# Kernel tuning notes

Measured on AMD Instinct MI355X. Metric: run time of the kernel, lower is better.

## Reference

```python
import jax, jax.numpy as jnp
import numpy as np

B, S, D = 2, 2048, 1024
H, DK = 16, 64  # n_heads, d_k == d_v


def setup_inputs() -> dict:
    key = jax.random.key(0)
    ks = jax.random.split(key, 12)
    sd = 1.0 / np.sqrt(D)
    inp = {
        "Q": jax.random.normal(ks[0], (B, S, D), jnp.float32),
        "K": jax.random.normal(ks[1], (B, S, D), jnp.float32),
        "V": jax.random.normal(ks[2], (B, S, D), jnp.float32),
        "attn_mask": jax.random.randint(ks[3], (B, S, S), 0, 2).astype(bool),
        "Wq": jax.random.normal(ks[4], (D, H * DK), jnp.float32) * sd,
        "bq": jnp.zeros((H * DK,), jnp.float32),
        "Wk": jax.random.normal(ks[5], (D, H * DK), jnp.float32) * sd,
        "bk": jnp.zeros((H * DK,), jnp.float32),
        "Wv": jax.random.normal(ks[6], (D, H * DK), jnp.float32) * sd,
        "bv": jnp.zeros((H * DK,), jnp.float32),
        "Wo": jax.random.normal(ks[7], (H * DK, D), jnp.float32) * sd,
        "bo": jnp.zeros((D,), jnp.float32),
        "ln_g": jnp.ones((D,), jnp.float32),
        "ln_b": jnp.zeros((D,), jnp.float32),
    }
    return inp


def _layer_norm(x, g, b, eps=1e-5):
    mu = jnp.mean(x, axis=-1, keepdims=True)
    var = jnp.var(x, axis=-1, keepdims=True)
    return (x - mu) * jax.lax.rsqrt(var + eps) * g + b


def reference(Q, K, V, attn_mask, Wq, bq, Wk, bk, Wv, bv, Wo, bo, ln_g, ln_b):
    # NOTE: faithful to the source — K and V projections are computed from Q.
    residual = Q
    q = (Q @ Wq + bq).reshape(B, S, H, DK).transpose(0, 2, 1, 3)  # [B,H,S,DK]
    k = (Q @ Wk + bk).reshape(B, S, H, DK).transpose(0, 2, 1, 3)
    v = (Q @ Wv + bv).reshape(B, S, H, DK).transpose(0, 2, 1, 3)
    scale = 1.0 / np.sqrt(DK)
    scores = jnp.einsum("bhqd,bhkd->bhqk", q, k) * scale  # [B,H,S,S]
    scores = jnp.where(attn_mask[:, None, :, :], jnp.float32(-1e9), scores)
    attn = jax.nn.softmax(scores, axis=-1)
    context = jnp.einsum("bhqk,bhkd->bhqd", attn, v)
    context = context.transpose(0, 2, 1, 3).reshape(B, S, H * DK)
    output = context @ Wo + bo
    return _layer_norm(output + residual, ln_g, ln_b), attn
```

## Files before the change

### kernel.cpp

```cpp
#include <hip/hip_runtime.h>
#include <stdint.h>

typedef unsigned short u16;
typedef short bf16x8 __attribute__((ext_vector_type(8)));
typedef float f32x4 __attribute__((ext_vector_type(4)));

static __device__ __forceinline__ u16 f2b(float f) {
    uint32_t u = __float_as_uint(f);
    uint32_t r = (u + 0x7fffu + ((u >> 16) & 1u)) >> 16;
    return (u16)r;
}
static __device__ __forceinline__ float b2f(u16 u) {
    union { float f; uint32_t i; } x; x.i = ((uint32_t)u) << 16; return x.f;
}

__global__ __launch_bounds__(256) void pack_mask_k(const int* __restrict__ mask,
                                                   unsigned long long* __restrict__ bits) {
    const int row = blockIdx.x;
    const int wave = threadIdx.x >> 6, lane = threadIdx.x & 63;
    const int* mrow = mask + (size_t)row * 2048;
#pragma unroll
    for (int it = 0; it < 8; ++it) {
        int col = it * 256 + threadIdx.x;
        unsigned long long b = __ballot(mrow[col] != 0);
        if (lane == 0) bits[(size_t)row * 32 + it * 4 + wave] = b;
    }
}

__global__ __launch_bounds__(256) void transpose_w_k(const float* __restrict__ Wq, const float* __restrict__ Wk,
                                                     const float* __restrict__ Wv, const float* __restrict__ Wo,
                                                     u16* __restrict__ WtAll) {
    __shared__ u16 t[32][36];
    const float* W = blockIdx.z == 0 ? Wq : blockIdx.z == 1 ? Wk : blockIdx.z == 2 ? Wv : Wo;
    u16* out = WtAll + (size_t)blockIdx.z * (1024u * 1024u);
    const int r = threadIdx.x >> 3, c4 = (threadIdx.x & 7) * 4;
    float4 v = *(const float4*)(W + (size_t)(blockIdx.y * 32 + r) * 1024 + blockIdx.x * 32 + c4);
    t[r][c4 + 0] = f2b(v.x); t[r][c4 + 1] = f2b(v.y); t[r][c4 + 2] = f2b(v.z); t[r][c4 + 3] = f2b(v.w);
    __syncthreads();
    ushort4 o;
    o.x = t[c4 + 0][r]; o.y = t[c4 + 1][r]; o.z = t[c4 + 2][r]; o.w = t[c4 + 3][r];
    *(ushort4*)(out + (size_t)(blockIdx.x * 32 + r) * 1024 + blockIdx.y * 32 + c4) = o;
}

__global__ __launch_bounds__(256) void proj_qkv_k(const float* __restrict__ Q, const u16* __restrict__ WtAll,
                                                  const float* __restrict__ bq, const float* __restrict__ bk,
                                                  const float* __restrict__ bv,
                                                  u16* __restrict__ q_ws, u16* __restrict__ k_ws,
                                                  u16* __restrict__ v_ws) {
    const int z = blockIdx.z;
    const u16* Bt = WtAll + (size_t)z * (1024u * 1024u);
    const float* bias = z == 0 ? bq : z == 1 ? bk : bv;
    u16* out = z == 0 ? q_ws : z == 1 ? k_ws : v_ws;
    const float oscale = (z == 0) ? 0.18033688011112042f : 1.0f;

    __shared__ u16 Asm[64][40];
    __shared__ u16 Bsm[64][40];

    const int tid = threadIdx.x;
    const int wave = tid >> 6, lane = tid & 63, quad = lane >> 4, l16 = lane & 15;
    const int m0 = blockIdx.y * 64, n0 = blockIdx.x * 64;
    const int srow = tid >> 2, scol = (tid & 3) * 8;

    const float* Ag = Q + (size_t)(m0 + srow) * 1024 + scol;
    const u16* Bg = Bt + (size_t)(n0 + srow) * 1024 + scol;

    const f32x4 zero = {0.f, 0.f, 0.f, 0.f};
    f32x4 acc[4];
#pragma unroll
    for (int i = 0; i < 4; ++i) acc[i] = zero;

    for (int k0 = 0; k0 < 1024; k0 += 32) {
        float4 a0 = *(const float4*)(Ag + k0);
        float4 a1 = *(const float4*)(Ag + k0 + 4);
        u16* asl = &Asm[srow][scol];
        asl[0] = f2b(a0.x); asl[1] = f2b(a0.y); asl[2] = f2b(a0.z); asl[3] = f2b(a0.w);
        asl[4] = f2b(a1.x); asl[5] = f2b(a1.y); asl[6] = f2b(a1.z); asl[7] = f2b(a1.w);
        *(bf16x8*)&Bsm[srow][scol] = *(const bf16x8*)(Bg + k0);
        __syncthreads();
        bf16x8 a = *(const bf16x8*)&Asm[wave * 16 + l16][quad * 8];
#pragma unroll
        for (int nt = 0; nt < 4; ++nt) {
            bf16x8 bb = *(const bf16x8*)&Bsm[nt * 16 + l16][quad * 8];
            acc[nt] = __builtin_amdgcn_mfma_f32_16x16x32_bf16(a, bb, acc[nt], 0, 0, 0);
        }
        __syncthreads();
    }

    const int h = blockIdx.x;
#pragma unroll
    for (int nt = 0; nt < 4; ++nt) {
        const int d = nt * 16 + l16;
        const float bsf = bias[h * 64 + d];
#pragma unroll
        for (int r = 0; r < 4; ++r) {
            const int m = m0 + wave * 16 + quad * 4 + r;
            const int bb = m >> 11, s = m & 2047;
            out[((size_t)(bb * 16 + h) * 2048 + s) * 64 + d] = f2b((acc[nt][r] + bsf) * oscale);
        }
    }
}

__global__ __launch_bounds__(256) void attn_k(const u16* __restrict__ q_ws, const u16* __restrict__ k_ws,
                                              const u16* __restrict__ v_ws,
                                              const unsigned long long* __restrict__ mbits,
                                              float* __restrict__ attn_out, u16* __restrict__ ctx_ws) {
    const int bh = blockIdx.y, b = bh >> 4, h = bh & 15;
    const int q0 = blockIdx.x * 64;
    const int tid = threadIdx.x;
    const int wave = tid >> 6, lane = tid & 63, quad = lane >> 4, l16 = lane & 15;

    __shared__ u16 Ksm[64][72];
    __shared__ u16 Vsm[64][72];
    __shared__ u16 Psm[4][16][72];

    const u16* qp = q_ws + ((size_t)bh * 2048 + q0 + wave * 16 + l16) * 64;
    const bf16x8 aq0 = *(const bf16x8*)(qp + quad * 8);
    const bf16x8 aq1 = *(const bf16x8*)(qp + 32 + quad * 8);

    const size_t mbase = ((size_t)b * 2048 + q0 + wave * 16 + quad * 4) * 32;

    const int r0 = tid >> 3, c0 = (tid & 7) * 8;
    const u16* kgb = k_ws + (size_t)bh * 2048 * 64;
    const u16* vgb = v_ws + (size_t)bh * 2048 * 64;

    const f32x4 zero = {0.f, 0.f, 0.f, 0.f};
    float lsum[4] = {0.f, 0.f, 0.f, 0.f};

    for (int kt = 0; kt < 32; ++kt) {
        const int s0 = kt * 64;
        *(bf16x8*)&Ksm[r0][c0] = *(const bf16x8*)(kgb + (size_t)(s0 + r0) * 64 + c0);
        *(bf16x8*)&Ksm[r0 + 32][c0] = *(const bf16x8*)(kgb + (size_t)(s0 + r0 + 32) * 64 + c0);
        __syncthreads();
        f32x4 sc[4];
#pragma unroll
        for (int nt = 0; nt < 4; ++nt) {
            sc[nt] = zero;
            bf16x8 bk0 = *(const bf16x8*)&Ksm[nt * 16 + l16][quad * 8];
            bf16x8 bk1 = *(const bf16x8*)&Ksm[nt * 16 + l16][32 + quad * 8];
            sc[nt] = __builtin_amdgcn_mfma_f32_16x16x32_bf16(aq0, bk0, sc[nt], 0, 0, 0);
            sc[nt] = __builtin_amdgcn_mfma_f32_16x16x32_bf16(aq1, bk1, sc[nt], 0, 0, 0);
        }
        unsigned long long mw[4];
#pragma unroll
        for (int r = 0; r < 4; ++r) mw[r] = mbits[mbase + (size_t)r * 32 + kt];
#pragma unroll
        for (int nt = 0; nt < 4; ++nt)
#pragma unroll
            for (int r = 0; r < 4; ++r) {
                const int bit = (int)((mw[r] >> (nt * 16 + l16)) & 1ull);
                lsum[r] += bit ? 0.f : exp2f(sc[nt][r]);
            }
        __syncthreads();
    }
#pragma unroll
    for (int r = 0; r < 4; ++r) {
#pragma unroll
        for (int off = 1; off < 16; off <<= 1) lsum[r] += __shfl_xor(lsum[r], off, 64);
    }
    float rl[4];
#pragma unroll
    for (int r = 0; r < 4; ++r) rl[r] = 1.0f / lsum[r];

    f32x4 cacc[4];
#pragma unroll
    for (int i = 0; i < 4; ++i) cacc[i] = zero;

    for (int kt = 0; kt < 32; ++kt) {
        const int s0 = kt * 64;
        *(bf16x8*)&Ksm[r0][c0] = *(const bf16x8*)(kgb + (size_t)(s0 + r0) * 64 + c0);
        *(bf16x8*)&Ksm[r0 + 32][c0] = *(const bf16x8*)(kgb + (size_t)(s0 + r0 + 32) * 64 + c0);
        bf16x8 v0 = *(const bf16x8*)(vgb + (size_t)(s0 + r0) * 64 + c0);
        bf16x8 v1 = *(const bf16x8*)(vgb + (size_t)(s0 + r0 + 32) * 64 + c0);
#pragma unroll
        for (int j = 0; j < 8; ++j) {
            Vsm[c0 + j][r0] = (u16)v0[j];
            Vsm[c0 + j][r0 + 32] = (u16)v1[j];
        }
        __syncthreads();

        f32x4 sc[4];
#pragma unroll
        for (int nt = 0; nt < 4; ++nt) {
            sc[nt] = zero;
            bf16x8 bk0 = *(const bf16x8*)&Ksm[nt * 16 + l16][quad * 8];
            bf16x8 bk1 = *(const bf16x8*)&Ksm[nt * 16 + l16][32 + quad * 8];
            sc[nt] = __builtin_amdgcn_mfma_f32_16x16x32_bf16(aq0, bk0, sc[nt], 0, 0, 0);
            sc[nt] = __builtin_amdgcn_mfma_f32_16x16x32_bf16(aq1, bk1, sc[nt], 0, 0, 0);
        }
        unsigned long long mw[4];
#pragma unroll
        for (int r = 0; r < 4; ++r) mw[r] = mbits[mbase + (size_t)r * 32 + kt];
#pragma unroll
        for (int nt = 0; nt < 4; ++nt)
#pragma unroll
            for (int r = 0; r < 4; ++r) {
                const int bit = (int)((mw[r] >> (nt * 16 + l16)) & 1ull);
                const float p = bit ? 0.f : exp2f(sc[nt][r]) * rl[r];
                Psm[wave][quad * 4 + r][nt * 16 + l16] = f2b(p);
            }
#pragma unroll
        for (int j = 0; j < 4; ++j) {
            const int pr = j * 4 + (lane >> 4), pc = (lane & 15) * 4;
            ushort4 pv = *(const ushort4*)&Psm[wave][pr][pc];
            float4 pf;
            pf.x = b2f(pv.x); pf.y = b2f(pv.y); pf.z = b2f(pv.z); pf.w = b2f(pv.w);
            float* ap = attn_out + ((size_t)bh * 2048 + q0 + wave * 16 + pr) * 2048 + s0 + pc;
            *(float4*)ap = pf;
        }
        bf16x8 pa0 = *(const bf16x8*)&Psm[wave][l16][quad * 8];
        bf16x8 pa1 = *(const bf16x8*)&Psm[wave][l16][32 + quad * 8];
#pragma unroll
        for (int dt = 0; dt < 4; ++dt) {
            bf16x8 bv0 = *(const bf16x8*)&Vsm[dt * 16 + l16][quad * 8];
            bf16x8 bv1 = *(const bf16x8*)&Vsm[dt * 16 + l16][32 + quad * 8];
            cacc[dt] = __builtin_amdgcn_mfma_f32_16x16x32_bf16(pa0, bv0, cacc[dt], 0, 0, 0);
            cacc[dt] = __builtin_amdgcn_mfma_f32_16x16x32_bf16(pa1, bv1, cacc[dt], 0, 0, 0);
        }
        __syncthreads();
    }

#pragma unroll
    for (int dt = 0; dt < 4; ++dt) {
        const int d = dt * 16 + l16;
#pragma unroll
        for (int r = 0; r < 4; ++r) {
            const int s = q0 + wave * 16 + quad * 4 + r;
            ctx_ws[((size_t)b * 2048 + s) * 1024 + h * 64 + d] = f2b(cacc[dt][r]);
        }
    }
}

__global__ __launch_bounds__(256) void out_proj_k(const u16* __restrict__ Ctx, const u16* __restrict__ WtO,
                                                  const float* __restrict__ bo, const float* __restrict__ Qin,
                                                  float* __restrict__ ln_in) {
    __shared__ u16 Asm[64][40];
    __shared__ u16 Bsm[64][40];
    const int tid = threadIdx.x;
    const int wave = tid >> 6, lane = tid & 63, quad = lane >> 4, l16 = lane & 15;
    const int m0 = blockIdx.y * 64, n0 = blockIdx.x * 64;
    const int srow = tid >> 2, scol = (tid & 3) * 8;
    const u16* Ag = Ctx + (size_t)(m0 + srow) * 1024 + scol;
    const u16* Bg = WtO + (size_t)(n0 + srow) * 1024 + scol;

    const f32x4 zero = {0.f, 0.f, 0.f, 0.f};
    f32x4 acc[4];
#pragma unroll
    for (int i = 0; i < 4; ++i) acc[i] = zero;

    for (int k0 = 0; k0 < 1024; k0 += 32) {
        *(bf16x8*)&Asm[srow][scol] = *(const bf16x8*)(Ag + k0);
        *(bf16x8*)&Bsm[srow][scol] = *(const bf16x8*)(Bg + k0);
        __syncthreads();
        bf16x8 a = *(const bf16x8*)&Asm[wave * 16 + l16][quad * 8];
#pragma unroll
        for (int nt = 0; nt < 4; ++nt) {
            bf16x8 bb = *(const bf16x8*)&Bsm[nt * 16 + l16][quad * 8];
            acc[nt] = __builtin_amdgcn_mfma_f32_16x16x32_bf16(a, bb, acc[nt], 0, 0, 0);
        }
        __syncthreads();
    }
#pragma unroll
    for (int nt = 0; nt < 4; ++nt) {
        const int n = n0 + nt * 16 + l16;
        const float bsf = bo[n];
#pragma unroll
        for (int r = 0; r < 4; ++r) {
            const int m = m0 + wave * 16 + quad * 4 + r;
            ln_in[(size_t)m * 1024 + n] = acc[nt][r] + bsf + Qin[(size_t)m * 1024 + n];
        }
    }
}

__global__ __launch_bounds__(256) void layernorm_k(const float* __restrict__ x, const float* __restrict__ g,
                                                   const float* __restrict__ bta, float* __restrict__ out) {
    const int row = blockIdx.x, tid = threadIdx.x;
    const float4 v = *(const float4*)(x + (size_t)row * 1024 + tid * 4);
    float s = v.x + v.y + v.z + v.w;
    float sq = v.x * v.x + v.y * v.y + v.z * v.z + v.w * v.w;
#pragma unroll
    for (int off = 32; off; off >>= 1) {
        s += __shfl_xor(s, off, 64);
        sq += __shfl_xor(sq, off, 64);
    }
    __shared__ float ss[4], ssq[4];
    const int wave = tid >> 6, lane = tid & 63;
    if (lane == 0) { ss[wave] = s; ssq[wave] = sq; }
    __syncthreads();
    const float S = ss[0] + ss[1] + ss[2] + ss[3];
    const float SQ = ssq[0] + ssq[1] + ssq[2] + ssq[3];
    const float mu = S * (1.f / 1024.f);
    const float rs = rsqrtf(SQ * (1.f / 1024.f) - mu * mu + 1e-5f);
    const float* vf = (const float*)&v;
    float4 o;
    float tmp[4];
#pragma unroll
    for (int j = 0; j < 4; ++j) {
        const int c = tid * 4 + j;
        tmp[j] = (vf[j] - mu) * rs * g[c] + bta[c];
    }
    o.x = tmp[0]; o.y = tmp[1]; o.z = tmp[2]; o.w = tmp[3];
    *(float4*)(out + (size_t)row * 1024 + tid * 4) = o;
}

extern "C" void kernel_launch(void* const* d_in, const int* in_sizes, int n_in,
                              void* d_out, int out_size, void* d_ws, size_t ws_size,
                              hipStream_t stream) {
    const float* Q  = (const float*)d_in[0];
    const int* mask = (const int*)d_in[3];
    const float* Wq = (const float*)d_in[4];
    const float* bq = (const float*)d_in[5];
    const float* Wk = (const float*)d_in[6];
    const float* bk = (const float*)d_in[7];
    const float* Wv = (const float*)d_in[8];
    const float* bv = (const float*)d_in[9];
    const float* Wo = (const float*)d_in[10];
    const float* bo = (const float*)d_in[11];
    const float* g  = (const float*)d_in[12];
    const float* be = (const float*)d_in[13];

    char* ws = (char*)d_ws;
    u16* WtAll = (u16*)(ws);
    u16* q_ws  = (u16*)(ws + ((size_t)8  << 20));
    u16* k_ws  = (u16*)(ws + ((size_t)16 << 20));
    u16* v_ws  = (u16*)(ws + ((size_t)24 << 20));
    u16* c_ws  = (u16*)(ws + ((size_t)32 << 20));
    float* ln_in = (float*)(ws + ((size_t)40 << 20));
    unsigned long long* mbits = (unsigned long long*)(ws + ((size_t)56 << 20));

    float* out_ln = (float*)d_out;
    float* out_at = (float*)d_out + (size_t)2 * 2048 * 1024;

    transpose_w_k<<<dim3(32, 32, 4), dim3(256), 0, stream>>>(Wq, Wk, Wv, Wo, WtAll);
    pack_mask_k<<<dim3(4096), dim3(256), 0, stream>>>(mask, mbits);
    proj_qkv_k<<<dim3(16, 64, 3), dim3(256), 0, stream>>>(Q, WtAll, bq, bk, bv, q_ws, k_ws, v_ws);
    attn_k<<<dim3(32, 32), dim3(256), 0, stream>>>(q_ws, k_ws, v_ws, mbits, out_at, c_ws);
    out_proj_k<<<dim3(16, 64), dim3(256), 0, stream>>>(c_ws, WtAll + (size_t)3 * 1024 * 1024, bo, Q, ln_in);
    layernorm_k<<<dim3(4096), dim3(256), 0, stream>>>(ln_in, g, be, out_ln);
    (void)in_sizes; (void)n_in; (void)out_size; (void)ws_size;
}
```

Measured before the change: 911.1 us.

## Use 128x128 GEMM tiles with direct global-to-LDS loads and pre-transposed V

Q is converted to bf16 once in a separate kernel. The QKV projection becomes one fused GEMM over the concatenated weights with 128x128 tiles, and both GEMMs load operands straight into LDS with global_load_lds. V is transposed in a dedicated kernel so the attention kernel can copy V tiles into LDS with vector stores instead of scattered per-element writes. This cuts global traffic and the fp32 conversion work inside the GEMM loops, at the cost of extra kernel launches and the workspace traffic for the intermediate buffers.

```diff
diff --git a/kernel.cpp b/kernel.cpp
--- a/kernel.cpp
+++ b/kernel.cpp
@@ -13,6 +13,11 @@
 static __device__ __forceinline__ float b2f(u16 u) {
     union { float f; uint32_t i; } x; x.i = ((uint32_t)u) << 16; return x.f;
 }
+
+#define GLOAD16(g, l)                                                        \
+    __builtin_amdgcn_global_load_lds(                                        \
+        (const __attribute__((address_space(1))) uint32_t*)(g),              \
+        (__attribute__((address_space(3))) uint32_t*)(l), 16, 0, 0)
 
 __global__ __launch_bounds__(256) void pack_mask_k(const int* __restrict__ mask,
                                                    unsigned long long* __restrict__ bits) {
@@ -42,66 +47,92 @@
     *(ushort4*)(out + (size_t)(blockIdx.x * 32 + r) * 1024 + blockIdx.y * 32 + c4) = o;
 }
 
-__global__ __launch_bounds__(256) void proj_qkv_k(const float* __restrict__ Q, const u16* __restrict__ WtAll,
+__global__ __launch_bounds__(256) void qcvt_k(const float* __restrict__ Q, u16* __restrict__ qbf) {
+    const size_t i = ((size_t)blockIdx.x * 256 + threadIdx.x) * 8;
+    float4 a = *(const float4*)(Q + i);
+    float4 b = *(const float4*)(Q + i + 4);
+    bf16x8 o;
+    o[0] = (short)f2b(a.x); o[1] = (short)f2b(a.y); o[2] = (short)f2b(a.z); o[3] = (short)f2b(a.w);
+    o[4] = (short)f2b(b.x); o[5] = (short)f2b(b.y); o[6] = (short)f2b(b.z); o[7] = (short)f2b(b.w);
+    *(bf16x8*)(qbf + i) = o;
+}
+
+__global__ __launch_bounds__(256) void gemm_qkv_k(const u16* __restrict__ Abf, const u16* __restrict__ WtAll,
                                                   const float* __restrict__ bq, const float* __restrict__ bk,
                                                   const float* __restrict__ bv,
                                                   u16* __restrict__ q_ws, u16* __restrict__ k_ws,
                                                   u16* __restrict__ v_ws) {
-    const int z = blockIdx.z;
-    const u16* Bt = WtAll + (size_t)z * (1024u * 1024u);
+    __shared__ u16 Asm[128 * 32];
+    __shared__ u16 Bsm[128 * 32];
+    const int tid = threadIdx.x;
+    const int wave = tid >> 6, lane = tid & 63, quad = lane >> 4, l16 = lane & 15;
+    const int wr = wave >> 1, wc = wave & 1;
+    const int m0 = blockIdx.y * 128, n0 = blockIdx.x * 128;
+
+    const u16* Ag = Abf + (size_t)(m0 + (tid >> 2)) * 1024 + (tid & 3) * 8;
+    const u16* Bg = WtAll + (size_t)(n0 + (tid >> 2)) * 1024 + (tid & 3) * 8;
+
+    const f32x4 zero = {0.f, 0.f, 0.f, 0.f};
+    f32x4 acc[4][4];
+#pragma unroll
+    for (int i = 0; i < 4; ++i)
+#pragma unroll
+        for (int j = 0; j < 4; ++j) acc[i][j] = zero;
+
+    for (int k0 = 0; k0 < 1024; k0 += 32) {
+        GLOAD16(Ag + k0, &Asm[tid * 8]);
+        GLOAD16(Ag + k0 + (size_t)64 * 1024, &Asm[2048 + tid * 8]);
+        GLOAD16(Bg + k0, &Bsm[tid * 8]);
+        GLOAD16(Bg + k0 + (size_t)64 * 1024, &Bsm[2048 + tid * 8]);
+        __syncthreads();
+        bf16x8 a[4], b[4];
+#pragma unroll
+        for (int i = 0; i < 4; ++i) {
+            a[i] = *(const bf16x8*)&Asm[(wr * 64 + i * 16 + l16) * 32 + quad * 8];
+            b[i] = *(const bf16x8*)&Bsm[(wc * 64 + i * 16 + l16) * 32 + quad * 8];
+        }
+#pragma unroll
+        for (int mi = 0; mi < 4; ++mi)
+#pragma unroll
+            for (int ni = 0; ni < 4; ++ni)
+                acc[mi][ni] = __builtin_amdgcn_mfma_f32_16x16x32_bf16(a[mi], b[ni], acc[mi][ni], 0, 0, 0);
+        __syncthreads();
+    }
+
+    const int z = n0 >> 10;
     const float* bias = z == 0 ? bq : z == 1 ? bk : bv;
     u16* out = z == 0 ? q_ws : z == 1 ? k_ws : v_ws;
     const float oscale = (z == 0) ? 0.18033688011112042f : 1.0f;
-
-    __shared__ u16 Asm[64][40];
-    __shared__ u16 Bsm[64][40];
-
-    const int tid = threadIdx.x;
-    const int wave = tid >> 6, lane = tid & 63, quad = lane >> 4, l16 = lane & 15;
-    const int m0 = blockIdx.y * 64, n0 = blockIdx.x * 64;
-    const int srow = tid >> 2, scol = (tid & 3) * 8;
-
-    const float* Ag = Q + (size_t)(m0 + srow) * 1024 + scol;
-    const u16* Bg = Bt + (size_t)(n0 + srow) * 1024 + scol;
-
-    const f32x4 zero = {0.f, 0.f, 0.f, 0.f};
-    f32x4 acc[4];
-#pragma unroll
-    for (int i = 0; i < 4; ++i) acc[i] = zero;
-
-    for (int k0 = 0; k0 < 1024; k0 += 32) {
-        float4 a0 = *(const float4*)(Ag + k0);
-        float4 a1 = *(const float4*)(Ag + k0 + 4);
-        u16* asl = &Asm[srow][scol];
-        asl[0] = f2b(a0.x); asl[1] = f2b(a0.y); asl[2] = f2b(a0.z); asl[3] = f2b(a0.w);
-        asl[4] = f2b(a1.x); asl[5] = f2b(a1.y); asl[6] = f2b(a1.z); asl[7] = f2b(a1.w);
-        *(bf16x8*)&Bsm[srow][scol] = *(const bf16x8*)(Bg + k0);
-        __syncthreads();
-        bf16x8 a = *(const bf16x8*)&Asm[wave * 16 + l16][quad * 8];
-#pragma unroll
-        for (int nt = 0; nt < 4; ++nt) {
-            bf16x8 bb = *(const bf16x8*)&Bsm[nt * 16 + l16][quad * 8];
-            acc[nt] = __builtin_amdgcn_mfma_f32_16x16x32_bf16(a, bb, acc[nt], 0, 0, 0);
-        }
-        __syncthreads();
-    }
-
-    const int h = blockIdx.x;
-#pragma unroll
-    for (int nt = 0; nt < 4; ++nt) {
-        const int d = nt * 16 + l16;
-        const float bsf = bias[h * 64 + d];
-#pragma unroll
-        for (int r = 0; r < 4; ++r) {
-            const int m = m0 + wave * 16 + quad * 4 + r;
-            const int bb = m >> 11, s = m & 2047;
-            out[((size_t)(bb * 16 + h) * 2048 + s) * 64 + d] = f2b((acc[nt][r] + bsf) * oscale);
-        }
-    }
+#pragma unroll
+    for (int ni = 0; ni < 4; ++ni) {
+        const int n = n0 + wc * 64 + ni * 16 + l16;
+        const int nn = n & 1023, h = nn >> 6, d = nn & 63;
+        const float bsf = bias[nn];
+#pragma unroll
+        for (int mi = 0; mi < 4; ++mi)
+#pragma unroll
+            for (int r = 0; r < 4; ++r) {
+                const int m = m0 + wr * 64 + mi * 16 + quad * 4 + r;
+                const int bb = m >> 11, s = m & 2047;
+                out[((size_t)(bb * 16 + h) * 2048 + s) * 64 + d] = f2b((acc[mi][ni][r] + bsf) * oscale);
+            }
+    }
+}
+
+__global__ __launch_bounds__(256) void vtr_k(const u16* __restrict__ v_ws, u16* __restrict__ vT) {
+    __shared__ u16 t[32][36];
+    const int bh = blockIdx.z, s0 = blockIdx.x * 32, d0 = blockIdx.y * 32;
+    const int r = threadIdx.x >> 3, c4 = (threadIdx.x & 7) * 4;
+    ushort4 v = *(const ushort4*)(v_ws + ((size_t)bh * 2048 + s0 + r) * 64 + d0 + c4);
+    t[r][c4 + 0] = v.x; t[r][c4 + 1] = v.y; t[r][c4 + 2] = v.z; t[r][c4 + 3] = v.w;
+    __syncthreads();
+    ushort4 o;
+    o.x = t[c4 + 0][r]; o.y = t[c4 + 1][r]; o.z = t[c4 + 2][r]; o.w = t[c4 + 3][r];
+    *(ushort4*)(vT + ((size_t)bh * 64 + d0 + r) * 2048 + s0 + c4) = o;
 }
 
 __global__ __launch_bounds__(256) void attn_k(const u16* __restrict__ q_ws, const u16* __restrict__ k_ws,
-                                              const u16* __restrict__ v_ws,
+                                              const u16* __restrict__ vT,
                                               const unsigned long long* __restrict__ mbits,
                                               float* __restrict__ attn_out, u16* __restrict__ ctx_ws) {
     const int bh = blockIdx.y, b = bh >> 4, h = bh & 15;
@@ -121,7 +152,7 @@
 
     const int r0 = tid >> 3, c0 = (tid & 7) * 8;
     const u16* kgb = k_ws + (size_t)bh * 2048 * 64;
-    const u16* vgb = v_ws + (size_t)bh * 2048 * 64;
+    const u16* vtg = vT + (size_t)bh * 64 * 2048;
 
     const f32x4 zero = {0.f, 0.f, 0.f, 0.f};
     float lsum[4] = {0.f, 0.f, 0.f, 0.f};
@@ -169,13 +200,8 @@
         const int s0 = kt * 64;
         *(bf16x8*)&Ksm[r0][c0] = *(const bf16x8*)(kgb + (size_t)(s0 + r0) * 64 + c0);
         *(bf16x8*)&Ksm[r0 + 32][c0] = *(const bf16x8*)(kgb + (size_t)(s0 + r0 + 32) * 64 + c0);
-        bf16x8 v0 = *(const bf16x8*)(vgb + (size_t)(s0 + r0) * 64 + c0);
-        bf16x8 v1 = *(const bf16x8*)(vgb + (size_t)(s0 + r0 + 32) * 64 + c0);
-#pragma unroll
-        for (int j = 0; j < 8; ++j) {
-            Vsm[c0 + j][r0] = (u16)v0[j];
-            Vsm[c0 + j][r0 + 32] = (u16)v1[j];
-        }
+        *(bf16x8*)&Vsm[r0][c0] = *(const bf16x8*)(vtg + (size_t)r0 * 2048 + s0 + c0);
+        *(bf16x8*)&Vsm[r0 + 32][c0] = *(const bf16x8*)(vtg + (size_t)(r0 + 32) * 2048 + s0 + c0);
         __syncthreads();
 
         f32x4 sc[4];
@@ -233,41 +259,53 @@
 __global__ __launch_bounds__(256) void out_proj_k(const u16* __restrict__ Ctx, const u16* __restrict__ WtO,
                                                   const float* __restrict__ bo, const float* __restrict__ Qin,
                                                   float* __restrict__ ln_in) {
-    __shared__ u16 Asm[64][40];
-    __shared__ u16 Bsm[64][40];
+    __shared__ u16 Asm[128 * 32];
+    __shared__ u16 Bsm[128 * 32];
     const int tid = threadIdx.x;
     const int wave = tid >> 6, lane = tid & 63, quad = lane >> 4, l16 = lane & 15;
-    const int m0 = blockIdx.y * 64, n0 = blockIdx.x * 64;
-    const int srow = tid >> 2, scol = (tid & 3) * 8;
-    const u16* Ag = Ctx + (size_t)(m0 + srow) * 1024 + scol;
-    const u16* Bg = WtO + (size_t)(n0 + srow) * 1024 + scol;
+    const int wr = wave >> 1, wc = wave & 1;
+    const int m0 = blockIdx.y * 128, n0 = blockIdx.x * 128;
+
+    const u16* Ag = Ctx + (size_t)(m0 + (tid >> 2)) * 1024 + (tid & 3) * 8;
+    const u16* Bg = WtO + (size_t)(n0 + (tid >> 2)) * 1024 + (tid & 3) * 8;
 
     const f32x4 zero = {0.f, 0.f, 0.f, 0.f};
-    f32x4 acc[4];
-#pragma unroll
-    for (int i = 0; i < 4; ++i) acc[i] = zero;
+    f32x4 acc[4][4];
+#pragma unroll
+    for (int i = 0; i < 4; ++i)
+#pragma unroll
+        for (int j = 0; j < 4; ++j) acc[i][j] = zero;
 
     for (int k0 = 0; k0 < 1024; k0 += 32) {
-        *(bf16x8*)&Asm[srow][scol] = *(const bf16x8*)(Ag + k0);
-        *(bf16x8*)&Bsm[srow][scol] = *(const bf16x8*)(Bg + k0);
-        __syncthreads();
-        bf16x8 a = *(const bf16x8*)&Asm[wave * 16 + l16][quad * 8];
-#pragma unroll
-        for (int nt = 0; nt < 4; ++nt) {
-            bf16x8 bb = *(const bf16x8*)&Bsm[nt * 16 + l16][quad * 8];
-            acc[nt] = __builtin_amdgcn_mfma_f32_16x16x32_bf16(a, bb, acc[nt], 0, 0, 0);
-        }
-        __syncthreads();
-    }
-#pragma unroll
-    for (int nt = 0; nt < 4; ++nt) {
-        const int n = n0 + nt * 16 + l16;
+        GLOAD16(Ag + k0, &Asm[tid * 8]);
+        GLOAD16(Ag + k0 + (size_t)64 * 1024, &Asm[2048 + tid * 8]);
+        GLOAD16(Bg + k0, &Bsm[tid * 8]);
+        GLOAD16(Bg + k0 + (size_t)64 * 1024, &Bsm[2048 + tid * 8]);
+        __syncthreads();
+        bf16x8 a[4], b[4];
+#pragma unroll
+        for (int i = 0; i < 4; ++i) {
+            a[i] = *(const bf16x8*)&Asm[(wr * 64 + i * 16 + l16) * 32 + quad * 8];
+            b[i] = *(const bf16x8*)&Bsm[(wc * 64 + i * 16 + l16) * 32 + quad * 8];
+        }
+#pragma unroll
+        for (int mi = 0; mi < 4; ++mi)
+#pragma unroll
+            for (int ni = 0; ni < 4; ++ni)
+                acc[mi][ni] = __builtin_amdgcn_mfma_f32_16x16x32_bf16(a[mi], b[ni], acc[mi][ni], 0, 0, 0);
+        __syncthreads();
+    }
+#pragma unroll
+    for (int ni = 0; ni < 4; ++ni) {
+        const int n = n0 + wc * 64 + ni * 16 + l16;
         const float bsf = bo[n];
 #pragma unroll
-        for (int r = 0; r < 4; ++r) {
-            const int m = m0 + wave * 16 + quad * 4 + r;
-            ln_in[(size_t)m * 1024 + n] = acc[nt][r] + bsf + Qin[(size_t)m * 1024 + n];
-        }
+        for (int mi = 0; mi < 4; ++mi)
+#pragma unroll
+            for (int r = 0; r < 4; ++r) {
+                const int m = m0 + wr * 64 + mi * 16 + quad * 4 + r;
+                ln_in[(size_t)m * 1024 + n] = acc[mi][ni][r] + bsf + Qin[(size_t)m * 1024 + n];
+            }
     }
 }
 
@@ -324,6 +362,8 @@
     u16* k_ws  = (u16*)(ws + ((size_t)16 << 20));
     u16* v_ws  = (u16*)(ws + ((size_t)24 << 20));
     u16* c_ws  = (u16*)(ws + ((size_t)32 << 20));
+    u16* qbf   = (u16*)(ws + ((size_t)40 << 20));
+    u16* vT    = (u16*)(ws + ((size_t)40 << 20));
     float* ln_in = (float*)(ws + ((size_t)40 << 20));
     unsigned long long* mbits = (unsigned long long*)(ws + ((size_t)56 << 20));
 
@@ -332,9 +372,11 @@
 
     transpose_w_k<<<dim3(32, 32, 4), dim3(256), 0, stream>>>(Wq, Wk, Wv, Wo, WtAll);
     pack_mask_k<<<dim3(4096), dim3(256), 0, stream>>>(mask, mbits);
-    proj_qkv_k<<<dim3(16, 64, 3), dim3(256), 0, stream>>>(Q, WtAll, bq, bk, bv, q_ws, k_ws, v_ws);
-    attn_k<<<dim3(32, 32), dim3(256), 0, stream>>>(q_ws, k_ws, v_ws, mbits, out_at, c_ws);
-    out_proj_k<<<dim3(16, 64), dim3(256), 0, stream>>>(c_ws, WtAll + (size_t)3 * 1024 * 1024, bo, Q, ln_in);
+    qcvt_k<<<dim3(2048), dim3(256), 0, stream>>>(Q, qbf);
+    gemm_qkv_k<<<dim3(24, 32), dim3(256), 0, stream>>>(qbf, WtAll, bq, bk, bv, q_ws, k_ws, v_ws);
+    vtr_k<<<dim3(64, 2, 32), dim3(256), 0, stream>>>(v_ws, vT);
+    attn_k<<<dim3(32, 32), dim3(256), 0, stream>>>(q_ws, k_ws, vT, mbits, out_at, c_ws);
+    out_proj_k<<<dim3(8, 32), dim3(256), 0, stream>>>(c_ws, WtAll + (size_t)3 * 1024 * 1024, bo, Q, ln_in);
     layernorm_k<<<dim3(4096), dim3(256), 0, stream>>>(ln_in, g, be, out_ln);
     (void)in_sizes; (void)n_in; (void)out_size; (void)ws_size;
 }
```

Result: faster. 837.5 us (-8.1%).
